# Kernel tuning notes

Hardware: AMD Instinct MI355X
Metric: run time of the kernel (lower is better)

Reference implementation:

```python
import jax, jax.numpy as jnp
import numpy as np

N_NODES = 50000
N_EDGES = 800000
D_FEAT = 128
N_HEADS = 4
HEAD_DIM = 32  # embed_dim 128 / 4 heads


def mish(x):
    return x * jnp.tanh(jax.nn.softplus(x))


def setup_inputs() -> dict:
    key = jax.random.key(0)
    ks = jax.random.split(key, 12)
    s = 1.0 / np.sqrt(D_FEAT)
    return {
        "nodes": jax.random.normal(ks[0], (N_NODES, D_FEAT), jnp.float32),
        "edges": jax.random.normal(ks[1], (N_EDGES, D_FEAT), jnp.float32),
        # DenseGeneral kernels [in, heads, head_dim], biases [heads, head_dim]
        "Ws_k": jax.random.normal(ks[2], (D_FEAT, N_HEADS, HEAD_DIM), jnp.float32) * s,
        "Ws_b": jnp.zeros((N_HEADS, HEAD_DIM), jnp.float32),
        "Wr_k": jax.random.normal(ks[3], (D_FEAT, N_HEADS, HEAD_DIM), jnp.float32) * s,
        "Wr_b": jnp.zeros((N_HEADS, HEAD_DIM), jnp.float32),
        "We_k": jax.random.normal(ks[4], (D_FEAT, N_HEADS, HEAD_DIM), jnp.float32) * s,
        "We_b": jnp.zeros((N_HEADS, HEAD_DIM), jnp.float32),
        # attention logit Dense(1): acts on last (head_dim) axis
        "attn_w": jax.random.normal(ks[5], (HEAD_DIM, 1), jnp.float32) / np.sqrt(HEAD_DIM),
        "attn_b": jnp.zeros((1,), jnp.float32),
        "senders": jax.random.randint(ks[6], (N_EDGES,), 0, N_NODES, jnp.int32),
        "receivers": jax.random.randint(ks[7], (N_EDGES,), 0, N_NODES, jnp.int32),
    }


def reference(nodes, edges, Ws_k, Ws_b, Wr_k, Wr_b, We_k, We_b, attn_w, attn_b,
              senders, receivers):
    n = nodes.shape[0]
    # update_edge_fn: W_s(nodes[senders]) + W_e(edges)   (no globals -> 0)
    sent = jnp.einsum('ef,fhd->ehd', nodes[senders], Ws_k) + Ws_b       # [E,H,D]
    e_att = sent + jnp.einsum('ef,fhd->ehd', edges, We_k) + We_b        # [E,H,D]
    # attention_logit_fn: Dense1(mish(edges + W_r(nodes[receivers])))
    recv = jnp.einsum('ef,fhd->ehd', nodes[receivers], Wr_k) + Wr_b     # [E,H,D]
    logits = jnp.einsum('ehd,do->eho', mish(e_att + recv), attn_w) + attn_b  # [E,H,1]
    # jraph.segment_softmax over receiver segments
    seg_max = jax.ops.segment_max(logits, receivers, num_segments=n)
    w = jnp.exp(logits - seg_max[receivers])
    denom = jax.ops.segment_sum(w, receivers, num_segments=n)
    w = w / denom[receivers]
    # attention_reduce_fn + segment_sum aggregation; node update = aggregated msgs
    msg = (w * e_att).reshape(e_att.shape[0], N_HEADS * HEAD_DIM)       # [E, H*D]
    out_nodes = jax.ops.segment_sum(msg, receivers, num_segments=n)     # [N, H*D]
    return out_nodes
```

## Files before the change

kernel.cpp:

```cpp
#include <hip/hip_runtime.h>
#include <hip/hip_bf16.h>

#define NN 50000
#define NE 800000
#define F 128
#define HD 128
#define H 4

typedef __attribute__((ext_vector_type(4))) float f32x4;
typedef __attribute__((ext_vector_type(8))) __bf16 bf16x8;
typedef __attribute__((ext_vector_type(2))) __bf16 bf16x2;


__device__ __forceinline__ float mish_f(float x) {
    if (x > 30.f) return x;
    float t = __expf(x);
    float u = 1.f + t;
    u = u * u;
    return x * (u - 1.f) * __builtin_amdgcn_rcpf(u + 1.f);
}

__device__ __forceinline__ unsigned pack2_bf16(float a, float b) {
    bf16x2 v;
    v.x = (__bf16)a;
    v.y = (__bf16)b;
    return __builtin_bit_cast(unsigned, v);
}
__device__ __forceinline__ float bf16lo_to_f32(unsigned p) {
    return __uint_as_float((p & 0xFFFFu) << 16);
}
__device__ __forceinline__ float bf16hi_to_f32(unsigned p) {
    return __uint_as_float(p & 0xFFFF0000u);
}

#define DPP_ADD(v, ctrl)                                                     \
    (v) += __int_as_float(__builtin_amdgcn_update_dpp(                       \
        0, __float_as_int(v), (ctrl), 0xf, 0xf, true))

__global__ __launch_bounds__(256) void prep_w(
    const float* __restrict__ W0, const float* __restrict__ W1,
    const float* __restrict__ W2, uint4* __restrict__ O,
    uint4* __restrict__ zero_dst)
{
    int b = blockIdx.x;
    if (b >= 3) {
        int i = (b - 3) * 256 + threadIdx.x;
        if (i < 25000) zero_dst[i] = make_uint4(0, 0, 0, 0);
        return;
    }
    const float* W = (b == 0) ? W0 : (b == 1) ? W1 : W2;
    uint4* out = O + b * 2048;
    for (int c = threadIdx.x; c < 2048; c += 256) {
        int fn = c >> 8, ks = (c >> 6) & 3, lane = c & 63;
        int lgp = lane >> 4, l15 = lane & 15;
        int col = fn * 16 + l15, k0 = ks * 32 + lgp * 8;
        unsigned u[4];
        #pragma unroll
        for (int i = 0; i < 4; ++i)
            u[i] = pack2_bf16(W[(k0 + 2 * i) * 128 + col],
                              W[(k0 + 2 * i + 1) * 128 + col]);
        out[c] = make_uint4(u[0], u[1], u[2], u[3]);
    }
}

__global__ __launch_bounds__(256) void hist_kernel(
    const int* __restrict__ receivers, unsigned* __restrict__ cnt)
{
    int i = blockIdx.x * 256 + threadIdx.x;
    if (i < NE) atomicAdd(&cnt[receivers[i]], 1u);
}

__global__ __launch_bounds__(256) void scan1_kernel(
    const unsigned* __restrict__ cnt, unsigned* __restrict__ rowptr,
    unsigned* __restrict__ bsum)
{
    __shared__ unsigned sh[256];
    const int t = threadIdx.x;
    int i = blockIdx.x * 256 + t;
    unsigned c = (i < NN) ? cnt[i] : 0u;
    sh[t] = c;
    __syncthreads();
    unsigned incl = c;
    for (int off = 1; off < 256; off <<= 1) {
        unsigned v = (t >= off) ? sh[t - off] : 0u;
        __syncthreads();
        incl += v;
        sh[t] = incl;
        __syncthreads();
    }
    if (i < NN) rowptr[i] = incl - c;
    if (t == 255) bsum[blockIdx.x] = incl;
}

__global__ __launch_bounds__(256) void scan3_kernel(
    unsigned* __restrict__ rowptr, const unsigned* __restrict__ bsum, int nb)
{
    __shared__ unsigned sh[256];
    __shared__ unsigned s_off;
    const int t = threadIdx.x;
    unsigned c = (t < nb) ? bsum[t] : 0u;
    sh[t] = c;
    __syncthreads();
    unsigned incl = c;
    for (int off = 1; off < 256; off <<= 1) {
        unsigned v = (t >= off) ? sh[t - off] : 0u;
        __syncthreads();
        incl += v;
        sh[t] = incl;
        __syncthreads();
    }
    if (t == 0) {
        s_off = (blockIdx.x > 0) ? sh[blockIdx.x - 1] : 0u;
        if (blockIdx.x == 0) rowptr[NN] = NE;
    }
    __syncthreads();
    int i = blockIdx.x * 256 + t;
    if (i < NN) rowptr[i] += s_off;
}

__global__ __launch_bounds__(256) void scatter_kernel(
    const int* __restrict__ receivers, const unsigned* __restrict__ rowptr,
    unsigned* __restrict__ cnt2, unsigned* __restrict__ jof)
{
    int i = blockIdx.x * 256 + threadIdx.x;
    if (i >= NE) return;
    int r = receivers[i];
    unsigned pos = rowptr[r] + atomicAdd(&cnt2[r], 1u);
    jof[i] = pos;
}

__global__ __launch_bounds__(256, 4) void proj_both(
    const float* __restrict__ X,
    const bf16x8* __restrict__ Wf0, const bf16x8* __restrict__ Wf1,
    const float* __restrict__ b0, const float* __restrict__ b1,
    int M, uint2* __restrict__ Sp, uint2* __restrict__ Rp)
{
    __shared__ __align__(16) char ldsA[32768];
    const int t = threadIdx.x;
    const int lane = t & 63;
    const int wid = t >> 6;
    const int wr = wid >> 1, wc = wid & 1;
    const int l15 = lane & 15, lgp = lane >> 4;
    const size_t rowbase = (size_t)blockIdx.x * 128;

    #pragma unroll
    for (int i = 0; i < 8; ++i) {
        int c = i * 256 + t;
        int row = c >> 4, cc = c & 15;
        size_t e = rowbase + row;
        uint4 p = make_uint4(0, 0, 0, 0);
        if (e < (size_t)M) {
            const float4* src = (const float4*)(X + e * F + cc * 8);
            float4 f0 = src[0], f1 = src[1];
            p.x = pack2_bf16(f0.x, f0.y);
            p.y = pack2_bf16(f0.z, f0.w);
            p.z = pack2_bf16(f1.x, f1.y);
            p.w = pack2_bf16(f1.z, f1.w);
        }
        unsigned byte = (unsigned)(row * 256 + cc * 16);
        byte ^= (unsigned)((row & 7) << 4);
        *(uint4*)(ldsA + byte) = p;
    }
    __syncthreads();

    #pragma unroll
    for (int pass = 0; pass < 2; ++pass) {
        const bf16x8* Wf = pass ? Wf1 : Wf0;
        const float* bias = pass ? b1 : b0;
        uint2* Y = pass ? Rp : Sp;

        f32x4 acc[4][4];
        #pragma unroll
        for (int n = 0; n < 4; ++n) {
            float bv = bias[wc * 64 + n * 16 + l15];
            #pragma unroll
            for (int m = 0; m < 4; ++m) {
                acc[m][n][0] = bv; acc[m][n][1] = bv;
                acc[m][n][2] = bv; acc[m][n][3] = bv;
            }
        }
        #pragma unroll
        for (int ks = 0; ks < 4; ++ks) {
            const int kb = ks * 64 + lgp * 16;
            bf16x8 af[4], bfr[4];
            #pragma unroll
            for (int m = 0; m < 4; ++m) {
                int row = wr * 64 + m * 16 + l15;
                unsigned byte = ((unsigned)(row * 256 + kb)) ^ ((row & 7) << 4);
                af[m] = *(const bf16x8*)(ldsA + byte);
            }
            #pragma unroll
            for (int n = 0; n < 4; ++n)
                bfr[n] = Wf[((wc * 4 + n) * 4 + ks) * 64 + lane];
            #pragma unroll
            for (int m = 0; m < 4; ++m)
                #pragma unroll
                for (int n = 0; n < 4; ++n)
                    acc[m][n] = __builtin_amdgcn_mfma_f32_16x16x32_bf16(
                        af[m], bfr[n], acc[m][n], 0, 0, 0);
        }
        #pragma unroll
        for (int m = 0; m < 4; ++m)
            #pragma unroll
            for (int j = 0; j < 4; ++j) {
                int row = wr * 64 + m * 16 + lgp * 4 + j;
                size_t e = rowbase + row;
                if (e >= (size_t)M) continue;
                uint2 pk;
                pk.x = pack2_bf16(acc[m][0][j], acc[m][1][j]);
                pk.y = pack2_bf16(acc[m][2][j], acc[m][3][j]);
                Y[e * 32 + l15 * 2 + wc] = pk;
            }
    }
}

__global__ __launch_bounds__(256, 8) void edge_gemm(
    const float* __restrict__ X, const bf16x8* __restrict__ Wf,
    const float* __restrict__ bias,
    const int* __restrict__ senders, const unsigned* __restrict__ jof,
    const uint4* __restrict__ Sp4, uint4* __restrict__ EAp)
{
    const int t = threadIdx.x;
    const int lane = t & 63;
    const int wid = t >> 6;
    const int l15 = lane & 15, lgp = lane >> 4;
    const size_t rowbase = (size_t)blockIdx.x * 64;
    const float* aptr = X + (rowbase + wid * 16 + l15) * F;

    f32x4 acc[8];
    #pragma unroll
    for (int n = 0; n < 8; ++n) {
        float bv = bias[n * 16 + l15];
        acc[n][0] = bv; acc[n][1] = bv; acc[n][2] = bv; acc[n][3] = bv;
    }

    #pragma unroll
    for (int ks = 0; ks < 4; ++ks) {
        const float4* ap = (const float4*)(aptr + ks * 32 + lgp * 8);
        float4 a0 = ap[0], a1 = ap[1];
        uint4 pu;
        pu.x = pack2_bf16(a0.x, a0.y);
        pu.y = pack2_bf16(a0.z, a0.w);
        pu.z = pack2_bf16(a1.x, a1.y);
        pu.w = pack2_bf16(a1.z, a1.w);
        bf16x8 af = __builtin_bit_cast(bf16x8, pu);
        #pragma unroll
        for (int n = 0; n < 8; ++n) {
            bf16x8 bfr = Wf[(n * 4 + ks) * 64 + lane];
            acc[n] = __builtin_amdgcn_mfma_f32_16x16x32_bf16(af, bfr, acc[n], 0, 0, 0);
        }
    }

    #pragma unroll
    for (int j = 0; j < 4; ++j) {
        int row = wid * 16 + lgp * 4 + j;
        size_t e = rowbase + row;
        int snd = senders[e];
        unsigned jj = jof[e];
        uint4 sv = Sp4[(size_t)snd * 16 + l15];
        unsigned uo[4];
        #pragma unroll
        for (int h = 0; h < 4; ++h) {
            unsigned sp = (h == 0) ? sv.x : (h == 1) ? sv.y : (h == 2) ? sv.z : sv.w;
            float elo = acc[2 * h][j]     + bf16lo_to_f32(sp);
            float ehi = acc[2 * h + 1][j] + bf16hi_to_f32(sp);
            uo[h] = pack2_bf16(elo, ehi);
        }
        EAp[(size_t)jj * 16 + l15] = make_uint4(uo[0], uo[1], uo[2], uo[3]);
    }
}

__global__ __launch_bounds__(256) void agg_kernel(
    const unsigned* __restrict__ rowptr,
    const unsigned* __restrict__ Rp32,
    const float* __restrict__ attw, const float* __restrict__ attb,
    const unsigned* __restrict__ EA, float* __restrict__ out)
{
    const int lane = threadIdx.x & 63;
    const int r = blockIdx.x * 4 + (threadIdx.x >> 6);
    if (r >= NN) return;
    const unsigned start = rowptr[r], end = rowptr[r + 1];

    const int h = lane >> 4;
    const int q = lane & 15;
    const int k = q * 4 + h;
    const int c0 = 32 * h + q;

    if (start == end) {
        out[(size_t)r * HD + c0]      = 0.f;
        out[(size_t)r * HD + c0 + 16] = 0.f;
        return;
    }

    unsigned rp = Rp32[(size_t)r * 64 + k];
    const float rlo = bf16lo_to_f32(rp), rhi = bf16hi_to_f32(rp);
    const float aw0 = attw[q];
    const float aw1 = attw[q + 16];
    const float ab0 = attb[0];
    const unsigned* ea = EA + k;

#define PROC(P, AX, AY, DN) do {                                             \
        float el_ = bf16lo_to_f32(P), eh_ = bf16hi_to_f32(P);                \
        float tt_ = mish_f(el_ + rlo) * aw0 + mish_f(eh_ + rhi) * aw1;       \
        DPP_ADD(tt_, 0xB1);  DPP_ADD(tt_, 0x4E);                             \
        DPP_ADD(tt_, 0x141); DPP_ADD(tt_, 0x140);                            \
        float w_ = __expf(tt_ + ab0);                                        \
        DN += w_; AX += w_ * el_; AY += w_ * eh_; } while (0)

    float ax0 = 0.f, ay0 = 0.f, dn0 = 0.f;
    float ax1 = 0.f, ay1 = 0.f, dn1 = 0.f;
    float ax2 = 0.f, ay2 = 0.f, dn2 = 0.f;
    float ax3 = 0.f, ay3 = 0.f, dn3 = 0.f;

    unsigned cnt = end - start;
    unsigned nq = cnt >> 2;
    unsigned j = start;
    if (nq) {
        const unsigned* e0 = ea + (size_t)start * 64;
        unsigned p0 = e0[0], p1 = e0[64], p2 = e0[128], p3 = e0[192];
        for (unsigned qq = 1; qq < nq; ++qq) {
            const unsigned* en = ea + (size_t)(start + qq * 4) * 64;
            unsigned n0 = en[0], n1 = en[64], n2 = en[128], n3 = en[192];
            PROC(p0, ax0, ay0, dn0);
            PROC(p1, ax1, ay1, dn1);
            PROC(p2, ax2, ay2, dn2);
            PROC(p3, ax3, ay3, dn3);
            p0 = n0; p1 = n1; p2 = n2; p3 = n3;
        }
        PROC(p0, ax0, ay0, dn0);
        PROC(p1, ax1, ay1, dn1);
        PROC(p2, ax2, ay2, dn2);
        PROC(p3, ax3, ay3, dn3);
        j = start + nq * 4;
    }
    for (; j < end; ++j) {
        unsigned p = ea[(size_t)j * 64];
        PROC(p, ax0, ay0, dn0);
    }
#undef PROC

    float rd = 1.f / (dn0 + dn1 + dn2 + dn3);
    out[(size_t)r * HD + c0]      = (ax0 + ax1 + ax2 + ax3) * rd;
    out[(size_t)r * HD + c0 + 16] = (ay0 + ay1 + ay2 + ay3) * rd;
}

extern "C" void kernel_launch(void* const* d_in, const int* in_sizes, int n_in,
                              void* d_out, int out_size, void* d_ws, size_t ws_size,
                              hipStream_t stream) {
    const float* nodes = (const float*)d_in[0];
    const float* edges = (const float*)d_in[1];
    const float* Ws_k  = (const float*)d_in[2];
    const float* Ws_b  = (const float*)d_in[3];
    const float* Wr_k  = (const float*)d_in[4];
    const float* Wr_b  = (const float*)d_in[5];
    const float* We_k  = (const float*)d_in[6];
    const float* We_b  = (const float*)d_in[7];
    const float* attw  = (const float*)d_in[8];
    const float* attb  = (const float*)d_in[9];
    const int* senders   = (const int*)d_in[10];
    const int* receivers = (const int*)d_in[11];
    float* out = (float*)d_out;

    char* ws = (char*)d_ws;
    const size_t CNT_OFF  = 0;
    const size_t CNT2_OFF = 200000;
    const size_t RP_OFF   = 400000;
    const size_t BS_OFF   = 600004;
    const size_t JOF_OFF  = 700000;
    const size_t WF_OFF   = 3900000;
    const size_t SP_OFF   = 4000000;
    const size_t RPP_OFF  = 16800000;
    const size_t EA_OFF   = 29600000;

    unsigned* cnt    = (unsigned*)(ws + CNT_OFF);
    unsigned* cnt2   = (unsigned*)(ws + CNT2_OFF);
    unsigned* rowptr = (unsigned*)(ws + RP_OFF);
    unsigned* bsum   = (unsigned*)(ws + BS_OFF);
    unsigned* jof    = (unsigned*)(ws + JOF_OFF);
    uint4*    Wf     = (uint4*)(ws + WF_OFF);
    uint2*    Sp     = (uint2*)(ws + SP_OFF);
    uint2*    Rp     = (uint2*)(ws + RPP_OFF);
    unsigned* EA     = (unsigned*)(ws + EA_OFF);
    (void)ws_size;

    const int NB = (NN + 255) / 256;

    prep_w<<<3 + 98, 256, 0, stream>>>(Ws_k, Wr_k, We_k, Wf, (uint4*)(ws + CNT_OFF));

    hist_kernel<<<(NE + 255) / 256, 256, 0, stream>>>(receivers, cnt);
    scan1_kernel<<<NB, 256, 0, stream>>>(cnt, rowptr, bsum);
    scan3_kernel<<<NB, 256, 0, stream>>>(rowptr, bsum, NB);
    scatter_kernel<<<(NE + 255) / 256, 256, 0, stream>>>(receivers, rowptr, cnt2, jof);

    proj_both<<<(NN + 127) / 128, 256, 0, stream>>>(
        nodes, (const bf16x8*)Wf, (const bf16x8*)(Wf + 2048),
        Ws_b, Wr_b, NN, Sp, Rp);

    edge_gemm<<<NE / 64, 256, 0, stream>>>(
        edges, (const bf16x8*)(Wf + 4096), We_b,
        senders, jof, (const uint4*)Sp, (uint4*)EA);

    agg_kernel<<<(NN + 3) / 4, 256, 0, stream>>>(
        rowptr, (const unsigned*)Rp, attw, attb, EA, out);
}
```

Before: 359.5 us.

## Compute attention logits in edge GEMM epilogue instead of aggregation kernel

Moves the mish and attention-logit computation from the per-receiver aggregation kernel into the edge GEMM epilogue. The epilogue now gathers the receiver projection, reduces per-head logits with DPP, and writes a per-edge float4 logit buffer in CSR order. The aggregation kernel then only loads the logits and applies exp, which shortens its per-edge dependency chain. The cost is an extra gather of the receiver projection per edge, an extra 12.8 MB logits write and read, and a lower occupancy hint on the GEMM kernel.

Measured after the change: 395.7 us. 1.1x slower.

```diff
diff --git a/kernel.cpp b/kernel.cpp
--- a/kernel.cpp
+++ b/kernel.cpp
@@ -36,6 +36,9 @@
 #define DPP_ADD(v, ctrl)                                                     \
     (v) += __int_as_float(__builtin_amdgcn_update_dpp(                       \
         0, __float_as_int(v), (ctrl), 0xf, 0xf, true))
+#define DPP_REDUCE16(v) do {                                                 \
+    DPP_ADD(v, 0xB1);  DPP_ADD(v, 0x4E);                                     \
+    DPP_ADD(v, 0x141); DPP_ADD(v, 0x140); } while (0)
 
 __global__ __launch_bounds__(256) void prep_w(
     const float* __restrict__ W0, const float* __restrict__ W1,
@@ -214,11 +217,14 @@
     }
 }
 
-__global__ __launch_bounds__(256, 8) void edge_gemm(
+__global__ __launch_bounds__(256, 6) void edge_gemm(
     const float* __restrict__ X, const bf16x8* __restrict__ Wf,
     const float* __restrict__ bias,
-    const int* __restrict__ senders, const unsigned* __restrict__ jof,
-    const uint4* __restrict__ Sp4, uint4* __restrict__ EAp)
+    const float* __restrict__ attw, const float* __restrict__ attb,
+    const int* __restrict__ senders, const int* __restrict__ receivers,
+    const unsigned* __restrict__ jof,
+    const uint4* __restrict__ Sp4, const uint4* __restrict__ Rp4,
+    uint4* __restrict__ EAp, float4* __restrict__ logits4)
 {
     const int t = threadIdx.x;
     const int lane = t & 63;
@@ -251,29 +257,61 @@
         }
     }
 
+    const float aw0 = attw[l15];
+    const float aw1 = attw[l15 + 16];
+    const float ab0 = attb[0];
     #pragma unroll
     for (int j = 0; j < 4; ++j) {
         int row = wid * 16 + lgp * 4 + j;
         size_t e = rowbase + row;
         int snd = senders[e];
+        int rcv = receivers[e];
         unsigned jj = jof[e];
         uint4 sv = Sp4[(size_t)snd * 16 + l15];
+        uint4 rv = Rp4[(size_t)rcv * 16 + l15];
         unsigned uo[4];
-        #pragma unroll
-        for (int h = 0; h < 4; ++h) {
-            unsigned sp = (h == 0) ? sv.x : (h == 1) ? sv.y : (h == 2) ? sv.z : sv.w;
-            float elo = acc[2 * h][j]     + bf16lo_to_f32(sp);
-            float ehi = acc[2 * h + 1][j] + bf16hi_to_f32(sp);
-            uo[h] = pack2_bf16(elo, ehi);
+        float ph0, ph1, ph2, ph3;
+        {
+            float elo = acc[0][j] + bf16lo_to_f32(sv.x);
+            float ehi = acc[1][j] + bf16hi_to_f32(sv.x);
+            uo[0] = pack2_bf16(elo, ehi);
+            ph0 = mish_f(elo + bf16lo_to_f32(rv.x)) * aw0
+                + mish_f(ehi + bf16hi_to_f32(rv.x)) * aw1;
+        }
+        {
+            float elo = acc[2][j] + bf16lo_to_f32(sv.y);
+            float ehi = acc[3][j] + bf16hi_to_f32(sv.y);
+            uo[1] = pack2_bf16(elo, ehi);
+            ph1 = mish_f(elo + bf16lo_to_f32(rv.y)) * aw0
+                + mish_f(ehi + bf16hi_to_f32(rv.y)) * aw1;
+        }
+        {
+            float elo = acc[4][j] + bf16lo_to_f32(sv.z);
+            float ehi = acc[5][j] + bf16hi_to_f32(sv.z);
+            uo[2] = pack2_bf16(elo, ehi);
+            ph2 = mish_f(elo + bf16lo_to_f32(rv.z)) * aw0
+                + mish_f(ehi + bf16hi_to_f32(rv.z)) * aw1;
+        }
+        {
+            float elo = acc[6][j] + bf16lo_to_f32(sv.w);
+            float ehi = acc[7][j] + bf16hi_to_f32(sv.w);
+            uo[3] = pack2_bf16(elo, ehi);
+            ph3 = mish_f(elo + bf16lo_to_f32(rv.w)) * aw0
+                + mish_f(ehi + bf16hi_to_f32(rv.w)) * aw1;
         }
         EAp[(size_t)jj * 16 + l15] = make_uint4(uo[0], uo[1], uo[2], uo[3]);
+        DPP_REDUCE16(ph0);
+        DPP_REDUCE16(ph1);
+        DPP_REDUCE16(ph2);
+        DPP_REDUCE16(ph3);
+        if (l15 == 0)
+            logits4[jj] = make_float4(ph0 + ab0, ph1 + ab0, ph2 + ab0, ph3 + ab0);
     }
 }
 
 __global__ __launch_bounds__(256) void agg_kernel(
     const unsigned* __restrict__ rowptr,
-    const unsigned* __restrict__ Rp32,
-    const float* __restrict__ attw, const float* __restrict__ attb,
+    const float* __restrict__ logits,
     const unsigned* __restrict__ EA, float* __restrict__ out)
 {
     const int lane = threadIdx.x & 63;
@@ -292,19 +330,12 @@
         return;
     }
 
-    unsigned rp = Rp32[(size_t)r * 64 + k];
-    const float rlo = bf16lo_to_f32(rp), rhi = bf16hi_to_f32(rp);
-    const float aw0 = attw[q];
-    const float aw1 = attw[q + 16];
-    const float ab0 = attb[0];
     const unsigned* ea = EA + k;
-
-#define PROC(P, AX, AY, DN) do {                                             \
+    const float* lg = logits + h;
+
+#define PROC(P, L, AX, AY, DN) do {                                          \
+        float w_ = __expf(L);                                                \
         float el_ = bf16lo_to_f32(P), eh_ = bf16hi_to_f32(P);                \
-        float tt_ = mish_f(el_ + rlo) * aw0 + mish_f(eh_ + rhi) * aw1;       \
-        DPP_ADD(tt_, 0xB1);  DPP_ADD(tt_, 0x4E);                             \
-        DPP_ADD(tt_, 0x141); DPP_ADD(tt_, 0x140);                            \
-        float w_ = __expf(tt_ + ab0);                                        \
         DN += w_; AX += w_ * el_; AY += w_ * eh_; } while (0)
 
     float ax0 = 0.f, ay0 = 0.f, dn0 = 0.f;
@@ -317,25 +348,31 @@
     unsigned j = start;
     if (nq) {
         const unsigned* e0 = ea + (size_t)start * 64;
+        const float* g0 = lg + (size_t)start * 4;
         unsigned p0 = e0[0], p1 = e0[64], p2 = e0[128], p3 = e0[192];
+        float l0 = g0[0], l1 = g0[4], l2 = g0[8], l3 = g0[12];
         for (unsigned qq = 1; qq < nq; ++qq) {
             const unsigned* en = ea + (size_t)(start + qq * 4) * 64;
+            const float* gn = lg + (size_t)(start + qq * 4) * 4;
             unsigned n0 = en[0], n1 = en[64], n2 = en[128], n3 = en[192];
-            PROC(p0, ax0, ay0, dn0);
-            PROC(p1, ax1, ay1, dn1);
-            PROC(p2, ax2, ay2, dn2);
-            PROC(p3, ax3, ay3, dn3);
+            float m0 = gn[0], m1 = gn[4], m2 = gn[8], m3 = gn[12];
+            PROC(p0, l0, ax0, ay0, dn0);
+            PROC(p1, l1, ax1, ay1, dn1);
+            PROC(p2, l2, ax2, ay2, dn2);
+            PROC(p3, l3, ax3, ay3, dn3);
             p0 = n0; p1 = n1; p2 = n2; p3 = n3;
-        }
-        PROC(p0, ax0, ay0, dn0);
-        PROC(p1, ax1, ay1, dn1);
-        PROC(p2, ax2, ay2, dn2);
-        PROC(p3, ax3, ay3, dn3);
+            l0 = m0; l1 = m1; l2 = m2; l3 = m3;
+        }
+        PROC(p0, l0, ax0, ay0, dn0);
+        PROC(p1, l1, ax1, ay1, dn1);
+        PROC(p2, l2, ax2, ay2, dn2);
+        PROC(p3, l3, ax3, ay3, dn3);
         j = start + nq * 4;
     }
     for (; j < end; ++j) {
         unsigned p = ea[(size_t)j * 64];
-        PROC(p, ax0, ay0, dn0);
+        float l = lg[(size_t)j * 4];
+        PROC(p, l, ax0, ay0, dn0);
     }
 #undef PROC
 
@@ -370,7 +407,8 @@
     const size_t WF_OFF   = 3900000;
     const size_t SP_OFF   = 4000000;
     const size_t RPP_OFF  = 16800000;
-    const size_t EA_OFF   = 29600000;
+    const size_t LG_OFF   = 29600000;
+    const size_t EA_OFF   = 42400000;
 
     unsigned* cnt    = (unsigned*)(ws + CNT_OFF);
     unsigned* cnt2   = (unsigned*)(ws + CNT2_OFF);
@@ -380,6 +418,7 @@
     uint4*    Wf     = (uint4*)(ws + WF_OFF);
     uint2*    Sp     = (uint2*)(ws + SP_OFF);
     uint2*    Rp     = (uint2*)(ws + RPP_OFF);
+    float*    logits = (float*)(ws + LG_OFF);
     unsigned* EA     = (unsigned*)(ws + EA_OFF);
     (void)ws_size;
 
@@ -398,8 +437,10 @@
 
     edge_gemm<<<NE / 64, 256, 0, stream>>>(
         edges, (const bf16x8*)(Wf + 4096), We_b,
-        senders, jof, (const uint4*)Sp, (uint4*)EA);
+        attw, attb, senders, receivers, jof,
+        (const uint4*)Sp, (const uint4*)Rp,
+        (uint4*)EA, (float4*)logits);
 
     agg_kernel<<<(NN + 3) / 4, 256, 0, stream>>>(
-        rowptr, (const unsigned*)Rp, attw, attb, EA, out);
-}
+        rowptr, logits, EA, out);
+}
```
